# Performance work log

Measured on AMD Instinct MI355X. Metric: run time of the kernel, lower is better.

Reference implementation:

```python
import jax, jax.numpy as jnp
import numpy as np

D = 768
H = 12
HD = D // H
FF = 3072
EPS = 1e-5


def layernorm(x, g, b):
    mu = jnp.mean(x, axis=-1, keepdims=True)
    var = jnp.mean(jnp.square(x - mu), axis=-1, keepdims=True)
    return (x - mu) * jax.lax.rsqrt(var + EPS) * g + b


def setup_inputs() -> dict:
    key = jax.random.key(0)
    ks = jax.random.split(key, 12)
    s = 0.02
    return {
        "x": jax.random.normal(ks[0], (4, 1024, D), dtype=jnp.float32),
        "w_qkv": jax.random.normal(ks[1], (D, 3 * D), dtype=jnp.float32) * s,
        "b_qkv": jnp.zeros((3 * D,), jnp.float32),
        "w_proj": jax.random.normal(ks[2], (D, D), dtype=jnp.float32) * s,
        "b_proj": jnp.zeros((D,), jnp.float32),
        "w1": jax.random.normal(ks[3], (D, FF), dtype=jnp.float32) * s,
        "b1": jnp.zeros((FF,), jnp.float32),
        "w2": jax.random.normal(ks[4], (FF, D), dtype=jnp.float32) * s,
        "b2": jnp.zeros((D,), jnp.float32),
        "g1": jnp.ones((D,), jnp.float32),
        "be1": jnp.zeros((D,), jnp.float32),
        "g2": jnp.ones((D,), jnp.float32),
        "be2": jnp.zeros((D,), jnp.float32),
    }


def reference(x, w_qkv, b_qkv, w_proj, b_proj, w1, b1, w2, b2, g1, be1, g2, be2):
    B, N, C = x.shape
    # --- attention (pre-norm) ---
    h = layernorm(x, g1, be1)
    qkv = (h @ w_qkv + b_qkv).reshape(B, N, 3, H, HD)
    q = jnp.transpose(qkv[:, :, 0], (0, 2, 1, 3))  # [B,H,N,hd]
    k = jnp.transpose(qkv[:, :, 1], (0, 2, 1, 3))
    v = jnp.transpose(qkv[:, :, 2], (0, 2, 1, 3))
    attn = jnp.einsum("bhqd,bhkd->bhqk", q, k) * (HD ** -0.5)
    attn = jax.nn.softmax(attn, axis=-1)
    o = jnp.einsum("bhqk,bhkd->bhqd", attn, v)
    o = jnp.transpose(o, (0, 2, 1, 3)).reshape(B, N, C)
    x = x + (o @ w_proj + b_proj)
    # --- feedforward (pre-norm) ---
    h2 = layernorm(x, g2, be2)
    ff = jax.nn.gelu(h2 @ w1 + b1, approximate=False) @ w2 + b2
    return x + ff
```

## Files before the change

### kernel.cpp

```cpp
#include <hip/hip_runtime.h>
#include <hip/hip_bf16.h>
#include <math.h>

typedef __attribute__((ext_vector_type(8))) short short8;
typedef __attribute__((ext_vector_type(4))) float f32x4;

#define DMODEL 768
#define THREE_D 2304
#define FFDIM 3072
#define NSEQ 1024
#define NHEAD 12
#define HEADD 64
#define MROWS 4096

__device__ __forceinline__ ushort f2bf(float f) {
  union { float f; unsigned u; } c; c.f = f;
  unsigned u = c.u;
  unsigned r = (u + 0x7fffu + ((u >> 16) & 1u)) >> 16;
  return (ushort)r;
}

__device__ __forceinline__ unsigned pack2bf(float a, float b) {
  union { __hip_bfloat162 h; unsigned u; } c;
  c.h = __float22bfloat162_rn(make_float2(a, b));
  return c.u;
}

__device__ __forceinline__ void load_lds16(const ushort* g, const ushort* l) {
  __builtin_amdgcn_global_load_lds(
      (const __attribute__((address_space(1))) unsigned int*)g,
      (__attribute__((address_space(3))) unsigned int*)l, 16, 0, 0);
}

template <int N> __device__ __forceinline__ void wait_vm() {
  if constexpr (N == 8)      asm volatile("s_waitcnt vmcnt(8)" ::: "memory");
  else if constexpr (N == 6) asm volatile("s_waitcnt vmcnt(6)" ::: "memory");
  else if constexpr (N == 4) asm volatile("s_waitcnt vmcnt(4)" ::: "memory");
  else                       asm volatile("s_waitcnt vmcnt(0)" ::: "memory");
}

__global__ __launch_bounds__(256) void ln_kernel(const float* __restrict__ x,
    const float* __restrict__ g, const float* __restrict__ be,
    ushort* __restrict__ out) {
  int row = blockIdx.x;
  const float* xr = x + (size_t)row * DMODEL;
  int tid = threadIdx.x;
  float v0 = xr[tid], v1 = xr[tid + 256], v2 = xr[tid + 512];
  __shared__ float red1[4], red2[4];
  float s = v0 + v1 + v2;
  #pragma unroll
  for (int off = 32; off; off >>= 1) s += __shfl_xor(s, off);
  if ((tid & 63) == 0) red1[tid >> 6] = s;
  __syncthreads();
  float mean = (red1[0] + red1[1] + red1[2] + red1[3]) * (1.0f / 768.0f);
  float d0 = v0 - mean, d1 = v1 - mean, d2 = v2 - mean;
  float q = d0 * d0 + d1 * d1 + d2 * d2;
  #pragma unroll
  for (int off = 32; off; off >>= 1) q += __shfl_xor(q, off);
  if ((tid & 63) == 0) red2[tid >> 6] = q;
  __syncthreads();
  float var = (red2[0] + red2[1] + red2[2] + red2[3]) * (1.0f / 768.0f);
  float rs = rsqrtf(var + 1e-5f);
  size_t base = (size_t)row * DMODEL;
  out[base + tid]       = f2bf(d0 * rs * g[tid]       + be[tid]);
  out[base + tid + 256] = f2bf(d1 * rs * g[tid + 256] + be[tid + 256]);
  out[base + tid + 512] = f2bf(d2 * rs * g[tid + 512] + be[tid + 512]);
}

__global__ void wt_all_kernel(
    const float* __restrict__ w_qkv, const float* __restrict__ w_proj,
    const float* __restrict__ w1, const float* __restrict__ w2,
    ushort* __restrict__ Wqkv_t, ushort* __restrict__ Wproj_t,
    ushort* __restrict__ W1_t, ushort* __restrict__ W2_t) {
  __shared__ float t[32][33];
  int id = blockIdx.x;
  const float* W; ushort* Wt; int K, N, bx, by;
  if (id < 1728)      { W = w_qkv;  Wt = Wqkv_t;  K = 768;  N = 2304; bx = id % 72; by = id / 72; }
  else if (id < 2304) { id -= 1728; W = w_proj; Wt = Wproj_t; K = 768;  N = 768;  bx = id % 24; by = id / 24; }
  else if (id < 4608) { id -= 2304; W = w1;     Wt = W1_t;    K = 768;  N = 3072; bx = id % 96; by = id / 96; }
  else                { id -= 4608; W = w2;     Wt = W2_t;    K = 3072; N = 768;  bx = id % 24; by = id / 24; }
  int n0 = bx * 32, k0 = by * 32;
  int tx = threadIdx.x, ty = threadIdx.y;
  #pragma unroll
  for (int r = 0; r < 4; r++)
    t[ty + r * 8][tx] = W[(size_t)(k0 + ty + r * 8) * N + n0 + tx];
  __syncthreads();
  #pragma unroll
  for (int r = 0; r < 4; r++)
    Wt[(size_t)(n0 + ty + r * 8) * K + k0 + tx] = f2bf(t[tx][ty + r * 8]);
}

__global__ void vt_kernel(const ushort* __restrict__ qkv, ushort* __restrict__ Vt) {
  __shared__ ushort t[32][33];
  int n0 = blockIdx.x * 32, d0 = blockIdx.y * 32, bh = blockIdx.z;
  int b = bh / NHEAD, hh = bh % NHEAD;
  int tx = threadIdx.x, ty = threadIdx.y;
  #pragma unroll
  for (int r = 0; r < 4; r++)
    t[ty + r * 8][tx] = qkv[(size_t)(b * NSEQ + n0 + ty + r * 8) * THREE_D +
                            2 * DMODEL + hh * HEADD + d0 + tx];
  __syncthreads();
  #pragma unroll
  for (int r = 0; r < 4; r++) {
    int n = n0 + tx;
    int np = (n & ~63) | (((n & 15) << 2) | ((n >> 4) & 3));
    Vt[((size_t)bh * HEADD + d0 + ty + r * 8) * NSEQ + np] = t[tx][ty + r * 8];
  }
}

template <int BN, int MODE>
__global__ __launch_bounds__(512, 2) void gemm256_kernel(
    const ushort* __restrict__ A, const ushort* __restrict__ Bt,
    const float* __restrict__ bias, void* __restrict__ Cout,
    int gx, int Ntot, int K) {
  constexpr int FN = BN / 64;
  constexpr int WN = BN / 4;
  constexpr int ABUF = (256 + BN) * 64;
  constexpr int BOFF = 256 * 64;
  __shared__ ushort S[2 * ABUF];
  int tid = threadIdx.x, lane = tid & 63, wave = tid >> 6;
  int wm = wave >> 2, wn = wave & 3;
  int rsel = lane & 15, quad = lane >> 4;
  int nwg = gridDim.x;
  int o = blockIdx.x;
  int wg = (o & 7) * (nwg >> 3) + (o >> 3);
  int bx = wg % gx, by = wg / gx;
  int m0 = by * 256, n0 = bx * BN;
  f32x4 acc[8][FN] = {};
  int xorc = (rsel & 7) * 8;

  auto SA = [&](int buf, int k0, int i) {
    int c0 = i * 512 + wave * 64;
    int c = c0 + lane, r = c >> 3;
    int kk = ((c ^ r) & 7) * 8;
    load_lds16(&A[(size_t)(m0 + r) * K + k0 + kk], S + buf * ABUF + c0 * 8);
  };
  auto SB = [&](int buf, int k0, int i) {
    int c0 = i * 512 + wave * 64;
    int c = c0 + lane, r = c >> 3;
    int kk = ((c ^ r) & 7) * 8;
    load_lds16(&Bt[(size_t)(n0 + r) * K + k0 + kk],
               S + buf * ABUF + BOFF + c0 * 8);
  };
  auto RDA = [&](int cur, int half, int ks, int mi) -> short8 {
    int R = wm * 128 + (half * 4 + mi) * 16 + rsel;
    return *(const short8*)&S[cur * ABUF + R * 64 + ((ks * 32 + quad * 8) ^ xorc)];
  };
  auto RDB = [&](int cur, int ks, int ni) -> short8 {
    int R = wn * WN + ni * 16 + rsel;
    return *(const short8*)&S[cur * ABUF + BOFF + R * 64 +
                              ((ks * 32 + quad * 8) ^ xorc)];
  };

  #pragma unroll
  for (int i = 0; i < 4; i++) SA(0, 0, i);
  #pragma unroll
  for (int i = 0; i < FN; i++) SB(0, 0, i);
  wait_vm<0>();
  __builtin_amdgcn_s_barrier();

  int ntk = K >> 6;
  for (int t = 0; t < ntk; t++) {
    int cur = t & 1, nxt = cur ^ 1;
    bool pre = (t + 1 < ntk);
    int nk0 = (t + 1) * 64;
    short8 afb[2][4], bfb[2][FN];
    #pragma unroll
    for (int mi = 0; mi < 4; mi++) afb[0][mi] = RDA(cur, 0, 0, mi);
    #pragma unroll
    for (int ni = 0; ni < FN; ni++) bfb[0][ni] = RDB(cur, 0, ni);
    #pragma unroll
    for (int p = 0; p < 4; p++) {
      const int ks = p >> 1, half = p & 1;
      if (p < 3) {
        const int ksn = (p + 1) >> 1, halfn = (p + 1) & 1;
        #pragma unroll
        for (int mi = 0; mi < 4; mi++)
          afb[(p + 1) & 1][mi] = RDA(cur, halfn, ksn, mi);
        if (p == 1) {
          #pragma unroll
          for (int ni = 0; ni < FN; ni++) bfb[1][ni] = RDB(cur, 1, ni);
        }
      }
      if (pre) {
        if (p == 0) {
          #pragma unroll
          for (int i = 0; i < FN; i++) SB(nxt, nk0, i);
          SA(nxt, nk0, 0);
        } else if (p == 1) {
          SA(nxt, nk0, 1); SA(nxt, nk0, 2); SA(nxt, nk0, 3);
        }
      }
      __builtin_amdgcn_s_setprio(1);
      #pragma unroll
      for (int mi = 0; mi < 4; mi++)
        #pragma unroll
        for (int ni = 0; ni < FN; ni++)
          acc[half * 4 + mi][ni] = __builtin_amdgcn_mfma_f32_16x16x32_bf16(
              afb[p & 1][mi], bfb[ks][ni], acc[half * 4 + mi][ni], 0, 0, 0);
      __builtin_amdgcn_s_setprio(0);
      __builtin_amdgcn_s_barrier();
    }
    wait_vm<0>();
    __builtin_amdgcn_s_barrier();
  }
  ushort* Cl = S;
  float bv[FN];
  #pragma unroll
  for (int ni = 0; ni < FN; ni++) bv[ni] = bias[n0 + wn * WN + ni * 16 + rsel];
  #pragma unroll
  for (int mi = 0; mi < 8; mi++) {
    int row = wm * 128 + mi * 16 + quad * 4;
    #pragma unroll
    for (int ni = 0; ni < FN; ni++) {
      int col = wn * WN + ni * 16 + rsel;
      #pragma unroll
      for (int j = 0; j < 4; j++) {
        float v = acc[mi][ni][j] + bv[ni];
        if (MODE == 2) v = 0.5f * v * (1.0f + erff(v * 0.70710678118654752f));
        Cl[(row + j) * 200 + col] = f2bf(v);
      }
    }
  }
  __syncthreads();
  constexpr int CPR = BN / 8;
  ushort* Cg = (ushort*)Cout;
  for (int c = tid; c < 256 * CPR; c += 512) {
    int row = c / CPR, off = c - row * CPR;
    int4 v = *(const int4*)&Cl[row * 200 + off * 8];
    *(int4*)&Cg[(size_t)(m0 + row) * Ntot + n0 + off * 8] = v;
  }
}

template <int BM, int BN>
__global__ __launch_bounds__(256) void gemm_kernel(
    const ushort* __restrict__ A, const ushort* __restrict__ Bt,
    const float* __restrict__ bias, const float* __restrict__ resid,
    float* __restrict__ Cout, int gx, int Ntot, int K) {
  constexpr int ABUF = (BM + BN) * 64;
  constexpr int BOFF = BM * 64;
  __shared__ ushort S[2 * ABUF];
  constexpr int WM = BM / 2, WN = BN / 2;
  constexpr int FM = WM / 16, FN = WN / 16;
  constexpr int NL = BM / 32 + BN / 32;
  int tid = threadIdx.x, lane = tid & 63, wave = tid >> 6;
  int wm = wave >> 1, wn = wave & 1;
  int rsel = lane & 15, quad = lane >> 4;
  int nwg = gridDim.x;
  int o = blockIdx.x;
  int wg = (o & 7) * (nwg >> 3) + (o >> 3);
  int bx = wg % gx, by = wg / gx;
  int m0 = by * BM, n0 = bx * BN;
  f32x4 acc[FM][FN] = {};

  auto STAGE = [&](int buf, int k0) {
    #pragma unroll
    for (int i = 0; i < BM / 32; i++) {
      int c0 = i * 256 + wave * 64;
      int c = c0 + lane, r = c >> 3;
      int kk = ((c ^ r) & 7) * 8;
      load_lds16(&A[(size_t)(m0 + r) * K + k0 + kk], S + buf * ABUF + c0 * 8);
    }
    #pragma unroll
    for (int i = 0; i < BN / 32; i++) {
      int c0 = i * 256 + wave * 64;
      int c = c0 + lane, r = c >> 3;
      int kk = ((c ^ r) & 7) * 8;
      load_lds16(&Bt[(size_t)(n0 + r) * K + k0 + kk],
                 S + buf * ABUF + BOFF + c0 * 8);
    }
  };

  STAGE(0, 0);
  int ntk = K >> 6;
  for (int t = 0; t < ntk; t++) {
    int cur = t & 1;
    if (t + 1 < ntk) {
      STAGE(cur ^ 1, (t + 1) * 64);
      wait_vm<NL>();
    } else {
      wait_vm<0>();
    }
    __builtin_amdgcn_s_barrier();
    short8 af[2][FM], bf[2][FN];
    #pragma unroll
    for (int ks = 0; ks < 2; ks++) {
      int ko = ks * 32 + quad * 8;
      #pragma unroll
      for (int mi = 0; mi < FM; mi++) {
        int R = wm * WM + mi * 16 + rsel;
        af[ks][mi] = *(const short8*)&S[cur * ABUF + R * 64 + (ko ^ ((R & 7) * 8))];
      }
      #pragma unroll
      for (int ni = 0; ni < FN; ni++) {
        int R = wn * WN + ni * 16 + rsel;
        bf[ks][ni] = *(const short8*)&S[cur * ABUF + BOFF + R * 64 + (ko ^ ((R & 7) * 8))];
      }
    }
    #pragma unroll
    for (int ks = 0; ks < 2; ks++)
      #pragma unroll
      for (int mi = 0; mi < FM; mi++)
        #pragma unroll
        for (int ni = 0; ni < FN; ni++)
          acc[mi][ni] = __builtin_amdgcn_mfma_f32_16x16x32_bf16(
              af[ks][mi], bf[ks][ni], acc[mi][ni], 0, 0, 0);
    asm volatile("s_waitcnt lgkmcnt(0)" ::: "memory");
    __builtin_amdgcn_s_barrier();
  }
  float* Cl = (float*)S;
  #pragma unroll
  for (int ni = 0; ni < FN; ni++) {
    int col = wn * WN + ni * 16 + rsel;
    float bvv = bias[n0 + col];
    #pragma unroll
    for (int mi = 0; mi < FM; mi++) {
      int row = wm * WM + mi * 16 + quad * 4;
      #pragma unroll
      for (int j = 0; j < 4; j++)
        Cl[(row + j) * 68 + col] = acc[mi][ni][j] + bvv;
    }
  }
  __syncthreads();
  constexpr int CPR = BN / 4;
  for (int c = tid; c < BM * CPR; c += 256) {
    int row = c / CPR, off = c - row * CPR;
    size_t gi = (size_t)(m0 + row) * Ntot + n0 + off * 4;
    float4 v = *(const float4*)&Cl[row * 68 + off * 4];
    float4 rr = *(const float4*)&resid[gi];
    v.x += rr.x; v.y += rr.y; v.z += rr.z; v.w += rr.w;
    *(float4*)&Cout[gi] = v;
  }
}

__global__ __launch_bounds__(256) void attn_kernel(
    const ushort* __restrict__ qkv, const ushort* __restrict__ Vt,
    ushort* __restrict__ o) {
  __shared__ ushort Klds[2][64][64];
  __shared__ ushort Vlds[2][64][64];
  __shared__ ushort Plds[4][16][72];
  const float CL2 = 0.18033688011112042f;
  int tid = threadIdx.x, lane = tid & 63, wave = tid >> 6;
  int qt = blockIdx.x, bh = blockIdx.y;
  int b = bh / NHEAD, hh = bh % NHEAD;
  int q0 = qt * 64;
  int rsel = lane & 15, quad = lane >> 4;
  int xorc = (rsel & 7) * 8;

  short8 qf[2];
  {
    int qrow = q0 + wave * 16 + rsel;
    const ushort* qp = qkv + (size_t)(b * NSEQ + qrow) * THREE_D + hh * HEADD + quad * 8;
    qf[0] = *(const short8*)qp;
    qf[1] = *(const short8*)(qp + 32);
  }
  short8 onesf;
  #pragma unroll
  for (int i = 0; i < 8; i++) onesf[i] = (short)0x3F80;

  int r0 = tid >> 3, d0 = (tid & 7) * 8;
  int c1 = tid + 256, r1 = c1 >> 3, d1 = (c1 & 7) * 8;
  int sw0 = d0 ^ ((r0 & 7) * 8), sw1 = d1 ^ ((r1 & 7) * 8);
  const ushort* Kg = qkv + (size_t)b * NSEQ * THREE_D + DMODEL + hh * HEADD;
  const ushort* Vg = Vt + (size_t)bh * HEADD * NSEQ;
  int4 kr0, kr1, vr0, vr1;
  auto LD = [&](int kv0) {
    kr0 = *(const int4*)&Kg[(size_t)(kv0 + r0) * THREE_D + d0];
    kr1 = *(const int4*)&Kg[(size_t)(kv0 + r1) * THREE_D + d1];
    vr0 = *(const int4*)&Vg[(size_t)r0 * NSEQ + kv0 + d0];
    vr1 = *(const int4*)&Vg[(size_t)r1 * NSEQ + kv0 + d1];
  };
  auto ST = [&](int bf) {
    *(int4*)&Klds[bf][r0][sw0] = kr0;
    *(int4*)&Klds[bf][r1][sw1] = kr1;
    *(int4*)&Vlds[bf][r0][sw0] = vr0;
    *(int4*)&Vlds[bf][r1][sw1] = vr1;
  };

  f32x4 oacc[4] = {};
  f32x4 osum = {};

  LD(0); ST(0); __syncthreads();

  for (int t = 0; t < 16; t++) {
    int bf = t & 1;
    if (t < 15) LD((t + 1) * 64);
    f32x4 sfr[4] = {};
    __builtin_amdgcn_s_setprio(1);
    #pragma unroll
    for (int ks = 0; ks < 2; ks++) {
      int ko = ks * 32 + quad * 8;
      #pragma unroll
      for (int nt = 0; nt < 4; nt++) {
        short8 kf = *(const short8*)&Klds[bf][nt * 16 + rsel][ko ^ xorc];
        sfr[nt] = __builtin_amdgcn_mfma_f32_16x16x32_bf16(qf[ks], kf, sfr[nt], 0, 0, 0);
      }
    }
    __builtin_amdgcn_s_setprio(0);
    #pragma unroll
    for (int i = 0; i < 4; i++) {
      float p0 = exp2f(fmaf(sfr[0][i], CL2, -12.0f));
      float p1 = exp2f(fmaf(sfr[1][i], CL2, -12.0f));
      float p2 = exp2f(fmaf(sfr[2][i], CL2, -12.0f));
      float p3 = exp2f(fmaf(sfr[3][i], CL2, -12.0f));
      uint2 pw = make_uint2(pack2bf(p0, p1), pack2bf(p2, p3));
      *(uint2*)&Plds[wave][quad * 4 + i][rsel * 4] = pw;
    }
    __builtin_amdgcn_s_setprio(1);
    #pragma unroll
    for (int ks = 0; ks < 2; ks++) {
      int ko = ks * 32 + quad * 8;
      short8 pf = *(const short8*)&Plds[wave][rsel][ko];
      #pragma unroll
      for (int nt = 0; nt < 4; nt++) {
        short8 vf = *(const short8*)&Vlds[bf][nt * 16 + rsel][ko ^ xorc];
        oacc[nt] = __builtin_amdgcn_mfma_f32_16x16x32_bf16(pf, vf, oacc[nt], 0, 0, 0);
      }
      osum = __builtin_amdgcn_mfma_f32_16x16x32_bf16(pf, onesf, osum, 0, 0, 0);
    }
    __builtin_amdgcn_s_setprio(0);
    if (t < 15) ST(bf ^ 1);
    __syncthreads();
  }
  float rin[4];
  #pragma unroll
  for (int i = 0; i < 4; i++) rin[i] = __builtin_amdgcn_rcpf(osum[i]);
  #pragma unroll
  for (int nt = 0; nt < 4; nt++)
    #pragma unroll
    for (int i = 0; i < 4; i++) {
      int qrow = q0 + wave * 16 + quad * 4 + i;
      int col = hh * HEADD + nt * 16 + rsel;
      o[(size_t)(b * NSEQ + qrow) * DMODEL + col] = f2bf(oacc[nt][i] * rin[i]);
    }
}

extern "C" void kernel_launch(void* const* d_in, const int* in_sizes, int n_in,
                              void* d_out, int out_size, void* d_ws, size_t ws_size,
                              hipStream_t stream) {
  const float* x      = (const float*)d_in[0];
  const float* w_qkv  = (const float*)d_in[1];
  const float* b_qkv  = (const float*)d_in[2];
  const float* w_proj = (const float*)d_in[3];
  const float* b_proj = (const float*)d_in[4];
  const float* w1     = (const float*)d_in[5];
  const float* b1     = (const float*)d_in[6];
  const float* w2     = (const float*)d_in[7];
  const float* b2     = (const float*)d_in[8];
  const float* g1     = (const float*)d_in[9];
  const float* be1    = (const float*)d_in[10];
  const float* g2     = (const float*)d_in[11];
  const float* be2    = (const float*)d_in[12];
  float* out = (float*)d_out;

  char* ws = (char*)d_ws;
  ushort* Wqkv_t  = (ushort*)(ws + 0);
  ushort* Wproj_t = (ushort*)(ws + 3538944);
  ushort* W1_t    = (ushort*)(ws + 4718592);
  ushort* W2_t    = (ushort*)(ws + 9437184);
  ushort* hbuf    = (ushort*)(ws + 14155776);
  ushort* qkv     = (ushort*)(ws + 20447232);
  ushort* ff1     = qkv;
  ushort* VtB     = (ushort*)(ws + 45613056);
  ushort* obuf    = (ushort*)(ws + 51904512);
  float*  x2      = (float*)(ws + 58195968);

  dim3 tb(32, 8);
  wt_all_kernel<<<6912, tb, 0, stream>>>(w_qkv, w_proj, w1, w2,
                                         Wqkv_t, Wproj_t, W1_t, W2_t);

  ln_kernel<<<MROWS, 256, 0, stream>>>(x, g1, be1, hbuf);

  gemm256_kernel<192, 0><<<192, 512, 0, stream>>>(
      hbuf, Wqkv_t, b_qkv, qkv, THREE_D / 192, THREE_D, DMODEL);

  vt_kernel<<<dim3(NSEQ / 32, HEADD / 32, 4 * NHEAD), tb, 0, stream>>>(qkv, VtB);

  attn_kernel<<<dim3(NSEQ / 64, 4 * NHEAD), 256, 0, stream>>>(qkv, VtB, obuf);

  gemm_kernel<128, 64><<<384, 256, 0, stream>>>(
      obuf, Wproj_t, b_proj, x, x2, DMODEL / 64, DMODEL, DMODEL);

  ln_kernel<<<MROWS, 256, 0, stream>>>(x2, g2, be2, hbuf);

  gemm256_kernel<192, 2><<<256, 512, 0, stream>>>(
      hbuf, W1_t, b1, ff1, FFDIM / 192, FFDIM, DMODEL);

  gemm_kernel<128, 64><<<384, 256, 0, stream>>>(
      ff1, W2_t, b2, x2, out, DMODEL / 64, DMODEL, FFDIM);

  (void)in_sizes; (void)n_in; (void)out_size; (void)ws_size;
}
```

Baseline: 156.3 us.

## Double attention query tile, widen projection GEMM tiles, drop inner-loop barrier

The attention kernel now processes 128 query rows per block, two 16-row slices per wave, so each K/V tile staged in LDS is reused twice as often, at the cost of more accumulator registers and half as many blocks. The two residual GEMMs switch from 128x64 to 128x128 tiles with 192 blocks, and their epilogue stride and LDS size are adjusted to fit the wider tile. One s_barrier inside the gemm256 k-loop is removed to cut synchronisation, which risks an LDS race if the staging order relied on it. The smaller grids may leave compute units idle on a large GPU.

```diff
diff --git a/kernel.cpp b/kernel.cpp
--- a/kernel.cpp
+++ b/kernel.cpp
@@ -199,7 +199,6 @@
           acc[half * 4 + mi][ni] = __builtin_amdgcn_mfma_f32_16x16x32_bf16(
               afb[p & 1][mi], bfb[ks][ni], acc[half * 4 + mi][ni], 0, 0, 0);
       __builtin_amdgcn_s_setprio(0);
-      __builtin_amdgcn_s_barrier();
     }
     wait_vm<0>();
     __builtin_amdgcn_s_barrier();
@@ -239,7 +238,10 @@
     float* __restrict__ Cout, int gx, int Ntot, int K) {
   constexpr int ABUF = (BM + BN) * 64;
   constexpr int BOFF = BM * 64;
-  __shared__ ushort S[2 * ABUF];
+  constexpr int CSTR = BN + 4;
+  constexpr int SMEM = (2 * ABUF * 2 > BM * CSTR * 4) ? 2 * ABUF
+                                                      : BM * CSTR * 2;
+  __shared__ ushort S[SMEM];
   constexpr int WM = BM / 2, WN = BN / 2;
   constexpr int FM = WM / 16, FN = WN / 16;
   constexpr int NL = BM / 32 + BN / 32;
@@ -318,7 +320,7 @@
       int row = wm * WM + mi * 16 + quad * 4;
       #pragma unroll
       for (int j = 0; j < 4; j++)
-        Cl[(row + j) * 68 + col] = acc[mi][ni][j] + bvv;
+        Cl[(row + j) * CSTR + col] = acc[mi][ni][j] + bvv;
     }
   }
   __syncthreads();
@@ -326,7 +328,7 @@
   for (int c = tid; c < BM * CPR; c += 256) {
     int row = c / CPR, off = c - row * CPR;
     size_t gi = (size_t)(m0 + row) * Ntot + n0 + off * 4;
-    float4 v = *(const float4*)&Cl[row * 68 + off * 4];
+    float4 v = *(const float4*)&Cl[row * CSTR + off * 4];
     float4 rr = *(const float4*)&resid[gi];
     v.x += rr.x; v.y += rr.y; v.z += rr.z; v.w += rr.w;
     *(float4*)&Cout[gi] = v;
@@ -338,21 +340,22 @@
     ushort* __restrict__ o) {
   __shared__ ushort Klds[2][64][64];
   __shared__ ushort Vlds[2][64][64];
-  __shared__ ushort Plds[4][16][72];
+  __shared__ ushort Plds[4][32][72];
   const float CL2 = 0.18033688011112042f;
   int tid = threadIdx.x, lane = tid & 63, wave = tid >> 6;
   int qt = blockIdx.x, bh = blockIdx.y;
   int b = bh / NHEAD, hh = bh % NHEAD;
-  int q0 = qt * 64;
+  int q0 = qt * 128;
   int rsel = lane & 15, quad = lane >> 4;
   int xorc = (rsel & 7) * 8;
 
-  short8 qf[2];
-  {
-    int qrow = q0 + wave * 16 + rsel;
+  short8 qf[2][2];
+  #pragma unroll
+  for (int qs = 0; qs < 2; qs++) {
+    int qrow = q0 + wave * 32 + qs * 16 + rsel;
     const ushort* qp = qkv + (size_t)(b * NSEQ + qrow) * THREE_D + hh * HEADD + quad * 8;
-    qf[0] = *(const short8*)qp;
-    qf[1] = *(const short8*)(qp + 32);
+    qf[qs][0] = *(const short8*)qp;
+    qf[qs][1] = *(const short8*)(qp + 32);
   }
   short8 onesf;
   #pragma unroll
@@ -377,15 +380,15 @@
     *(int4*)&Vlds[bf][r1][sw1] = vr1;
   };
 
-  f32x4 oacc[4] = {};
-  f32x4 osum = {};
+  f32x4 oacc[2][4] = {};
+  f32x4 osum2[2] = {};
 
   LD(0); ST(0); __syncthreads();
 
   for (int t = 0; t < 16; t++) {
     int bf = t & 1;
     if (t < 15) LD((t + 1) * 64);
-    f32x4 sfr[4] = {};
+    f32x4 sfr[2][4] = {};
     __builtin_amdgcn_s_setprio(1);
     #pragma unroll
     for (int ks = 0; ks < 2; ks++) {
@@ -393,46 +396,57 @@
       #pragma unroll
       for (int nt = 0; nt < 4; nt++) {
         short8 kf = *(const short8*)&Klds[bf][nt * 16 + rsel][ko ^ xorc];
-        sfr[nt] = __builtin_amdgcn_mfma_f32_16x16x32_bf16(qf[ks], kf, sfr[nt], 0, 0, 0);
+        #pragma unroll
+        for (int qs = 0; qs < 2; qs++)
+          sfr[qs][nt] = __builtin_amdgcn_mfma_f32_16x16x32_bf16(
+              qf[qs][ks], kf, sfr[qs][nt], 0, 0, 0);
       }
     }
     __builtin_amdgcn_s_setprio(0);
     #pragma unroll
-    for (int i = 0; i < 4; i++) {
-      float p0 = exp2f(fmaf(sfr[0][i], CL2, -12.0f));
-      float p1 = exp2f(fmaf(sfr[1][i], CL2, -12.0f));
-      float p2 = exp2f(fmaf(sfr[2][i], CL2, -12.0f));
-      float p3 = exp2f(fmaf(sfr[3][i], CL2, -12.0f));
-      uint2 pw = make_uint2(pack2bf(p0, p1), pack2bf(p2, p3));
-      *(uint2*)&Plds[wave][quad * 4 + i][rsel * 4] = pw;
-    }
+    for (int qs = 0; qs < 2; qs++)
+      #pragma unroll
+      for (int i = 0; i < 4; i++) {
+        float p0 = exp2f(fmaf(sfr[qs][0][i], CL2, -12.0f));
+        float p1 = exp2f(fmaf(sfr[qs][1][i], CL2, -12.0f));
+        float p2 = exp2f(fmaf(sfr[qs][2][i], CL2, -12.0f));
+        float p3 = exp2f(fmaf(sfr[qs][3][i], CL2, -12.0f));
+        uint2 pw = make_uint2(pack2bf(p0, p1), pack2bf(p2, p3));
+        *(uint2*)&Plds[wave][qs * 16 + quad * 4 + i][rsel * 4] = pw;
+      }
     __builtin_amdgcn_s_setprio(1);
     #pragma unroll
     for (int ks = 0; ks < 2; ks++) {
       int ko = ks * 32 + quad * 8;
-      short8 pf = *(const short8*)&Plds[wave][rsel][ko];
+      short8 pf0 = *(const short8*)&Plds[wave][rsel][ko];
+      short8 pf1 = *(const short8*)&Plds[wave][16 + rsel][ko];
       #pragma unroll
       for (int nt = 0; nt < 4; nt++) {
         short8 vf = *(const short8*)&Vlds[bf][nt * 16 + rsel][ko ^ xorc];
-        oacc[nt] = __builtin_amdgcn_mfma_f32_16x16x32_bf16(pf, vf, oacc[nt], 0, 0, 0);
-      }
-      osum = __builtin_amdgcn_mfma_f32_16x16x32_bf16(pf, onesf, osum, 0, 0, 0);
+        oacc[0][nt] = __builtin_amdgcn_mfma_f32_16x16x32_bf16(pf0, vf, oacc[0][nt], 0, 0, 0);
+        oacc[1][nt] = __builtin_amdgcn_mfma_f32_16x16x32_bf16(pf1, vf, oacc[1][nt], 0, 0, 0);
+      }
+      osum2[0] = __builtin_amdgcn_mfma_f32_16x16x32_bf16(pf0, onesf, osum2[0], 0, 0, 0);
+      osum2[1] = __builtin_amdgcn_mfma_f32_16x16x32_bf16(pf1, onesf, osum2[1], 0, 0, 0);
     }
     __builtin_amdgcn_s_setprio(0);
     if (t < 15) ST(bf ^ 1);
     __syncthreads();
   }
-  float rin[4];
-  #pragma unroll
-  for (int i = 0; i < 4; i++) rin[i] = __builtin_amdgcn_rcpf(osum[i]);
-  #pragma unroll
-  for (int nt = 0; nt < 4; nt++)
-    #pragma unroll
-    for (int i = 0; i < 4; i++) {
-      int qrow = q0 + wave * 16 + quad * 4 + i;
-      int col = hh * HEADD + nt * 16 + rsel;
-      o[(size_t)(b * NSEQ + qrow) * DMODEL + col] = f2bf(oacc[nt][i] * rin[i]);
-    }
+  #pragma unroll
+  for (int qs = 0; qs < 2; qs++) {
+    float rin[4];
+    #pragma unroll
+    for (int i = 0; i < 4; i++) rin[i] = __builtin_amdgcn_rcpf(osum2[qs][i]);
+    #pragma unroll
+    for (int nt = 0; nt < 4; nt++)
+      #pragma unroll
+      for (int i = 0; i < 4; i++) {
+        int qrow = q0 + wave * 32 + qs * 16 + quad * 4 + i;
+        int col = hh * HEADD + nt * 16 + rsel;
+        o[(size_t)(b * NSEQ + qrow) * DMODEL + col] = f2bf(oacc[qs][nt][i] * rin[i]);
+      }
+  }
 }
 
 extern "C" void kernel_launch(void* const* d_in, const int* in_sizes, int n_in,
@@ -476,18 +490,18 @@
 
   vt_kernel<<<dim3(NSEQ / 32, HEADD / 32, 4 * NHEAD), tb, 0, stream>>>(qkv, VtB);
 
-  attn_kernel<<<dim3(NSEQ / 64, 4 * NHEAD), 256, 0, stream>>>(qkv, VtB, obuf);
-
-  gemm_kernel<128, 64><<<384, 256, 0, stream>>>(
-      obuf, Wproj_t, b_proj, x, x2, DMODEL / 64, DMODEL, DMODEL);
+  attn_kernel<<<dim3(NSEQ / 128, 4 * NHEAD), 256, 0, stream>>>(qkv, VtB, obuf);
+
+  gemm_kernel<128, 128><<<192, 256, 0, stream>>>(
+      obuf, Wproj_t, b_proj, x, x2, DMODEL / 128, DMODEL, DMODEL);
 
   ln_kernel<<<MROWS, 256, 0, stream>>>(x2, g2, be2, hbuf);
 
   gemm256_kernel<192, 2><<<256, 512, 0, stream>>>(
       hbuf, W1_t, b1, ff1, FFDIM / 192, FFDIM, DMODEL);
 
-  gemm_kernel<128, 64><<<384, 256, 0, stream>>>(
-      ff1, W2_t, b2, x2, out, DMODEL / 64, DMODEL, FFDIM);
+  gemm_kernel<128, 128><<<192, 256, 0, stream>>>(
+      ff1, W2_t, b2, x2, out, DMODEL / 128, DMODEL, FFDIM);
 
   (void)in_sizes; (void)n_in; (void)out_size; (void)ws_size;
 }
```

Measured after the change: 170.8 us. 9.3% more time.
